# Kernel tuning notes

Measured on AMD Instinct MI355X. Metric: run time of the kernel, lower is better.

Reference implementation:

```python
import jax, jax.numpy as jnp
import numpy as np

N_STEPS = 5
N_ETYPES = 4
N_GRAPHS = 64
HEADS = 2
N, E, D = 50000, 600000, 128
C = 32


def setup_inputs() -> dict:
    key = jax.random.key(0)
    ks = jax.random.split(key, 24)
    s = 0.08  # param scale to keep activations well-conditioned
    return {
        "in_feat1": jax.random.normal(ks[0], (N, D), jnp.float32),
        "in_feat2": jax.random.normal(ks[1], (N, D), jnp.float32),
        "src1": jax.random.randint(ks[2], (E,), 0, N, jnp.int32),
        "dst1": jax.random.randint(ks[3], (E,), 0, N, jnp.int32),
        "etype1": jax.random.randint(ks[4], (E,), 0, N_ETYPES, jnp.int32),
        "gid1": jnp.sort(jax.random.randint(ks[5], (N,), 0, N_GRAPHS, jnp.int32)),
        "src2": jax.random.randint(ks[6], (E,), 0, N, jnp.int32),
        "dst2": jax.random.randint(ks[7], (E,), 0, N, jnp.int32),
        "etype2": jax.random.randint(ks[8], (E,), 0, N_ETYPES, jnp.int32),
        "gid2": jnp.sort(jax.random.randint(ks[9], (N,), 0, N_GRAPHS, jnp.int32)),
        "W_et": jax.random.normal(ks[10], (N_ETYPES, D, D), jnp.float32) * s,
        "b_et": jax.random.normal(ks[11], (N_ETYPES, D), jnp.float32) * s,
        "W_ih": jax.random.normal(ks[12], (3 * D, D), jnp.float32) * s,
        "W_hh": jax.random.normal(ks[13], (3 * D, D), jnp.float32) * s,
        "b_ih": jax.random.normal(ks[14], (3 * D,), jnp.float32) * s,
        "b_hh": jax.random.normal(ks[15], (3 * D,), jnp.float32) * s,
        "W_fc": jax.random.normal(ks[16], (HEADS * D, D), jnp.float32) * s,
        "attn_l": jax.random.normal(ks[17], (HEADS, D), jnp.float32) * s,
        "attn_r": jax.random.normal(ks[18], (HEADS, D), jnp.float32) * s,
        "gat_bias": jax.random.normal(ks[19], (HEADS * D,), jnp.float32) * s,
        "W_cls": jax.random.normal(ks[20], (C, D), jnp.float32) * s,
        "b_cls": jax.random.normal(ks[21], (C,), jnp.float32) * s,
    }


def _ggann(feat, src, dst, etype, gid,
           W_et, b_et, W_ih, W_hh, b_ih, b_hh,
           W_fc, attn_l, attn_r, gat_bias, W_cls, b_cls):
    n = feat.shape[0]
    h = feat  # in_feats == out_feats -> no zero-padding needed
    # ---- GatedGraphConv: n_steps of per-etype message passing + GRU ----
    for _ in range(N_STEPS):
        # per-etype linear on all nodes: [K, N, D]
        t = jnp.einsum('kod,nd->kno', W_et, h) + b_et[:, None, :]
        msg = t[etype, src]                         # [E, D] gather by (etype, src)
        a = jax.ops.segment_sum(msg, dst, num_segments=n)  # [N, D]
        # GRUCell(a, h)
        gi = a @ W_ih.T + b_ih                      # [N, 3D]
        gh = h @ W_hh.T + b_hh
        i_r, i_z, i_n = jnp.split(gi, 3, axis=1)
        h_r, h_z, h_n = jnp.split(gh, 3, axis=1)
        r = jax.nn.sigmoid(i_r + h_r)
        z = jax.nn.sigmoid(i_z + h_z)
        nn_ = jnp.tanh(i_n + r * h_n)
        h = (1.0 - z) * nn_ + z * h
    # F.normalize (L2 over dim=1) then sigmoid
    h = h / jnp.maximum(jnp.linalg.norm(h, axis=1, keepdims=True), 1e-12)
    h = jax.nn.sigmoid(h)
    # ---- GATConv (num_heads=2) ----
    zft = (h @ W_fc.T).reshape(n, HEADS, D)         # [N, H, D]
    el = jnp.sum(zft * attn_l[None], axis=-1)       # [N, H]
    er = jnp.sum(zft * attn_r[None], axis=-1)
    e = jax.nn.leaky_relu(el[src] + er[dst], 0.2)   # [E, H]
    m = jax.ops.segment_max(e, dst, num_segments=n)
    ex = jnp.exp(e - m[dst])
    den = jax.ops.segment_sum(ex, dst, num_segments=n)
    alpha = ex / den[dst]                           # edge softmax per dst, per head
    rst = jax.ops.segment_sum(alpha[:, :, None] * zft[src], dst, num_segments=n)
    rst = rst + gat_bias.reshape(1, HEADS, D)
    h = jax.nn.relu(rst)                            # [N, H, D] (dropout = eval identity)
    # ---- mean_nodes per graph + classify ----
    sums = jax.ops.segment_sum(h, gid, num_segments=N_GRAPHS)      # [B, H, D]
    cnt = jax.ops.segment_sum(jnp.ones((n, 1, 1), h.dtype), gid, num_segments=N_GRAPHS)
    hg = sums / jnp.maximum(cnt, 1.0)
    return hg @ W_cls.T + b_cls                     # [B, H, C]


def reference(in_feat1, in_feat2, src1, dst1, etype1, gid1,
              src2, dst2, etype2, gid2,
              W_et, b_et, W_ih, W_hh, b_ih, b_hh,
              W_fc, attn_l, attn_r, gat_bias, W_cls, b_cls):
    params = (W_et, b_et, W_ih, W_hh, b_ih, b_hh,
              W_fc, attn_l, attn_r, gat_bias, W_cls, b_cls)
    h1 = _ggann(in_feat1, src1, dst1, etype1, gid1, *params)  # [B, H, C]
    h2 = _ggann(in_feat2, src2, dst2, etype2, gid2, *params)
    # F.pairwise_distance(p=2, eps=1e-6) over last dim -> [B, H]
    dist = jnp.linalg.norm(h1 - h2 + 1e-6, axis=-1)
    return jax.nn.softmax(dist, axis=1)             # softmax over the 2 heads
```

## Files before the change

### kernel.cpp

```cpp
#include <hip/hip_runtime.h>
#include <math.h>

#define D 128
#define NG 64
#define NG2 128
#define NSTEPS 5

using short8 = __attribute__((ext_vector_type(8))) short;
using f32x4  = __attribute__((ext_vector_type(4))) float;
using f32x2  = __attribute__((ext_vector_type(2))) float;

__device__ __forceinline__ float sigf(float x) {
  float e = __expf(-fabsf(x));
  float inv = __fdividef(1.f, 1.f + e);
  return x >= 0.f ? inv : e * inv;
}
__device__ __forceinline__ float tanhf_fast(float x) {
  float e = __expf(-2.f * fabsf(x));
  float r = (1.f - e) * __fdividef(1.f, 1.f + e);
  return x >= 0.f ? r : -r;
}
__device__ __forceinline__ float lrelu(float x) { return x > 0.f ? x : 0.2f * x; }
__device__ __forceinline__ short f2bf(float x) {
  unsigned u = __float_as_uint(x);
  u += 0x7fff + ((u >> 16) & 1);
  return (short)(u >> 16);
}
__device__ __forceinline__ unsigned pk2(float x, float y) {
  return ((unsigned)(unsigned short)f2bf(y) << 16) | (unsigned short)f2bf(x);
}
__device__ __forceinline__ float bflo(unsigned v) { return __uint_as_float(v << 16); }
__device__ __forceinline__ float bfhi(unsigned v) { return __uint_as_float(v & 0xffff0000u); }
__device__ __forceinline__ float bf2f(short s) {
  return __uint_as_float(((unsigned)(unsigned short)s) << 16);
}
__device__ __forceinline__ unsigned char f2fp8(float x) {
  int p = __builtin_amdgcn_cvt_pk_fp8_f32(x, x, 0, false);
  return (unsigned char)(p & 0xff);
}

__device__ __forceinline__ void packK128(const float* __restrict__ W,
                                         short* __restrict__ P, int i) {
  int j = i & 7;
  int lane = (i >> 3) & 63;
  int kt = (i >> 9) & 3;
  int nt = i >> 11;
  int c = nt * 16 + (lane & 15);
  int k = kt * 32 + ((lane >> 4) << 3) + j;
  P[i] = f2bf(W[c * 128 + k]);
}
__device__ __forceinline__ void packA512f(const float* __restrict__ W_et,
                                          short* __restrict__ P, int i) {
  int j = i & 7;
  int lane = (i >> 3) & 63;
  int kt = (i >> 9) & 15;
  int nt = i >> 13;
  int c = nt * 16 + (lane & 15);
  int k = kt * 32 + ((lane >> 4) << 3) + j;
  P[i] = f2bf(W_et[(k >> 7) * 16384 + c * 128 + (k & 127)]);
}

__global__ __launch_bounds__(256) void k_setup(const float* __restrict__ W_et,
    const float* __restrict__ W_ih, const float* __restrict__ W_hh,
    const float* __restrict__ W_fc, const float* __restrict__ f1,
    const float* __restrict__ f2, short* __restrict__ WaP, short* __restrict__ WihP,
    short* __restrict__ WhhP, short* __restrict__ WfcP, short* __restrict__ hb,
    unsigned char* __restrict__ hq,
    int* __restrict__ deg, int* __restrict__ gcnt, int N2, int Nd4) {
  const int sA = 65536, sB = 49152, sC = 49152, sD = 32768;
  int sE = N2, sF = NG2;
  long sG = 2L * Nd4;
  long tot = (long)(sA + sB + sC + sD) + sE + sF + sG;
  for (long ii = (long)blockIdx.x * blockDim.x + threadIdx.x; ii < tot;
       ii += (long)gridDim.x * blockDim.x) {
    long r = ii;
    if (r < sA) { packA512f(W_et, WaP, (int)r); continue; }
    r -= sA;
    if (r < sB) { packK128(W_ih, WihP, (int)r); continue; }
    r -= sB;
    if (r < sC) { packK128(W_hh, WhhP, (int)r); continue; }
    r -= sC;
    if (r < sD) { packK128(W_fc, WfcP, (int)r); continue; }
    r -= sD;
    if (r < sE) { deg[r] = 0; continue; }
    r -= sE;
    if (r < sF) { gcnt[r] = 0; continue; }
    r -= sF;
    {
      int i = (int)r;
      float4 v = (i < Nd4) ? ((const float4*)f1)[i] : ((const float4*)f2)[i - Nd4];
      ((uint2*)hb)[i] = make_uint2(pk2(v.x, v.y), pk2(v.z, v.w));
      int q = __builtin_amdgcn_cvt_pk_fp8_f32(v.x, v.y, 0, false);
      q = __builtin_amdgcn_cvt_pk_fp8_f32(v.z, v.w, q, true);
      ((unsigned*)hq)[i] = (unsigned)q;
    }
  }
}

__global__ __launch_bounds__(256) void k_histgid(const int* __restrict__ dst1,
    const int* __restrict__ dst2, const int* __restrict__ gid1,
    const int* __restrict__ gid2, int E, int N, int* __restrict__ deg,
    int* __restrict__ gidc, int* __restrict__ gcnt, int EB, int N2) {
  __shared__ int cnt[NG2];
  if ((int)blockIdx.x < EB) {
    int slice = blockIdx.x & 7;
    int bls = blockIdx.x >> 3;
    int nbs = EB >> 3;
    int W = (N2 + 7) >> 3;
    int lo = slice * W, hi = lo + W;
    for (int e = bls * 256 + threadIdx.x; e < 2 * E; e += nbs * 256) {
      int d = (e < E) ? dst1[e] : dst2[e - E] + N;
      if (d >= lo && d < hi) atomicAdd(&deg[d], 1);
    }
  } else {
    int t = threadIdx.x;
    if (t < NG2) cnt[t] = 0;
    __syncthreads();
    int i = (blockIdx.x - EB) * 256 + t;
    if (i < 2 * N) {
      int g = (i < N) ? gid1[i] : gid2[i - N] + NG;
      gidc[i] = g;
      atomicAdd(&cnt[g], 1);
    }
    __syncthreads();
    if (t < NG2 && cnt[t]) atomicAdd(&gcnt[t], cnt[t]);
  }
}

__global__ __launch_bounds__(256) void k_scan_a(const int* __restrict__ deg, int n,
                                                int* __restrict__ bsum) {
  int base = blockIdx.x * 1024 + threadIdx.x * 4;
  int s = 0;
  if (base + 3 < n) {
    int4 v = *(const int4*)(deg + base);
    s = v.x + v.y + v.z + v.w;
  } else {
    for (int k = 0; k < 4; ++k) if (base + k < n) s += deg[base + k];
  }
  #pragma unroll
  for (int off = 32; off; off >>= 1) s += __shfl_xor(s, off);
  __shared__ int ws[4];
  if ((threadIdx.x & 63) == 0) ws[threadIdx.x >> 6] = s;
  __syncthreads();
  if (threadIdx.x == 0) bsum[blockIdx.x] = ws[0] + ws[1] + ws[2] + ws[3];
}

__global__ __launch_bounds__(1024) void k_scan_b(const int* __restrict__ bsum,
                                                 int* __restrict__ boffs, int nb) {
  int tid = threadIdx.x;
  int v = (tid < nb) ? bsum[tid] : 0;
  int lane = tid & 63, wv = tid >> 6;
  int x = v;
  #pragma unroll
  for (int off = 1; off < 64; off <<= 1) {
    int y = __shfl_up(x, off);
    if (lane >= off) x += y;
  }
  __shared__ int wsum[16];
  if (lane == 63) wsum[wv] = x;
  __syncthreads();
  if (tid < 16) {
    int u = wsum[tid];
    #pragma unroll
    for (int off = 1; off < 16; off <<= 1) {
      int y = __shfl_up(u, off);
      if (tid >= off) u += y;
    }
    wsum[tid] = u;
  }
  __syncthreads();
  int woff = wv ? wsum[wv - 1] : 0;
  if (tid < nb) boffs[tid] = woff + x - v;
}

__global__ __launch_bounds__(256) void k_scan_c(const int* __restrict__ deg,
    const int* __restrict__ boffs, int* __restrict__ row_ofs,
    int* __restrict__ cursor, int n) {
  int base = blockIdx.x * 1024 + threadIdx.x * 4;
  int v[4] = {0, 0, 0, 0};
  if (base + 3 < n) {
    int4 t = *(const int4*)(deg + base);
    v[0] = t.x; v[1] = t.y; v[2] = t.z; v[3] = t.w;
  } else {
    for (int k = 0; k < 4; ++k) if (base + k < n) v[k] = deg[base + k];
  }
  int s = v[0] + v[1] + v[2] + v[3];
  int lane = threadIdx.x & 63, wv = threadIdx.x >> 6;
  int x = s;
  #pragma unroll
  for (int off = 1; off < 64; off <<= 1) {
    int y = __shfl_up(x, off);
    if (lane >= off) x += y;
  }
  __shared__ int wsum[4];
  if (lane == 63) wsum[wv] = x;
  __syncthreads();
  int woff = 0;
  for (int w = 0; w < wv; ++w) woff += wsum[w];
  int run = boffs[blockIdx.x] + woff + x - s;
  #pragma unroll
  for (int k = 0; k < 4; ++k) {
    int i = base + k;
    if (i < n) {
      cursor[i] = run;
      run += v[k];
      row_ofs[i + 1] = run;
    }
  }
  if (blockIdx.x == 0 && threadIdx.x == 0) row_ofs[0] = 0;
}

__global__ __launch_bounds__(256) void k_scatter(const int* __restrict__ src1,
    const int* __restrict__ dst1, const int* __restrict__ ety1,
    const int* __restrict__ src2, const int* __restrict__ dst2,
    const int* __restrict__ ety2, int E, int N, int* __restrict__ cursor,
    int* __restrict__ csr_se, int N2) {
  int slice = blockIdx.x & 7;
  int bls = blockIdx.x >> 3;
  int nbs = gridDim.x >> 3;
  int W = (N2 + 7) >> 3;
  int lo = slice * W, hi = lo + W;
  for (int e = bls * 256 + threadIdx.x; e < 2 * E; e += nbs * 256) {
    int d = (e < E) ? dst1[e] : dst2[e - E] + N;
    if (d < lo || d >= hi) continue;
    int s, et;
    if (e < E) { s = src1[e]; et = ety1[e]; }
    else { s = src2[e - E] + N; et = ety2[e - E]; }
    int p = atomicAdd(&cursor[d], 1);
    csr_se[p] = (s << 10) + et;
  }
}

__global__ __launch_bounds__(1024) void k_aggemm(const unsigned char* __restrict__ hq,
    const int* __restrict__ row_ofs, const int* __restrict__ csr_se,
    const short* __restrict__ WaP, const float* __restrict__ b_et,
    short* __restrict__ ab, int M) {
  __shared__ short Stile[16 * 512];
  __shared__ float lcnt[16][4];
  int tid = threadIdx.x;
  int lane = tid & 63, wave = tid >> 6;
  int row0 = blockIdx.x * 16;

  int li = wave;
  int node = row0 + li;
  f32x2 A0 = {0.f, 0.f}, A1 = {0.f, 0.f}, A2 = {0.f, 0.f}, A3 = {0.f, 0.f};
  int c0 = 0, c1 = 0, c2 = 0, c3 = 0;
  const char* hqb = (const char*)hq;
  if (node < M) {
    int beg = row_ofs[node], end = row_ofs[node + 1];
    #define ACC(ET, V) do { \
        f32x2 t_ = __builtin_amdgcn_cvt_pk_f32_fp8((unsigned)(V), false); \
        if (ET == 0)      { A0 += t_; ++c0; } \
        else if (ET == 1) { A1 += t_; ++c1; } \
        else if (ET == 2) { A2 += t_; ++c2; } \
        else              { A3 += t_; ++c3; } } while (0)
    for (int base = beg; base < end; base += 64) {
      int nv = end - base; if (nv > 64) nv = 64;
      int r = (lane < nv) ? csr_se[base + lane] : 0;
      int j = 0;
      for (; j + 16 <= nv; j += 16) {
        int rr[16];
        #pragma unroll
        for (int k = 0; k < 16; ++k) rr[k] = __builtin_amdgcn_readlane(r, j + k);
        unsigned short v[16];
        #pragma unroll
        for (int k = 0; k < 16; ++k)
          v[k] = ((const unsigned short*)(hqb + (rr[k] >> 3)))[lane];
        #pragma unroll
        for (int k = 0; k < 16; ++k) ACC(rr[k] & 3, v[k]);
      }
      for (; j + 8 <= nv; j += 8) {
        int rr[8];
        #pragma unroll
        for (int k = 0; k < 8; ++k) rr[k] = __builtin_amdgcn_readlane(r, j + k);
        unsigned short v[8];
        #pragma unroll
        for (int k = 0; k < 8; ++k)
          v[k] = ((const unsigned short*)(hqb + (rr[k] >> 3)))[lane];
        #pragma unroll
        for (int k = 0; k < 8; ++k) ACC(rr[k] & 3, v[k]);
      }
      for (; j + 4 <= nv; j += 4) {
        int rr[4];
        #pragma unroll
        for (int k = 0; k < 4; ++k) rr[k] = __builtin_amdgcn_readlane(r, j + k);
        unsigned short v[4];
        #pragma unroll
        for (int k = 0; k < 4; ++k)
          v[k] = ((const unsigned short*)(hqb + (rr[k] >> 3)))[lane];
        #pragma unroll
        for (int k = 0; k < 4; ++k) ACC(rr[k] & 3, v[k]);
      }
      for (; j < nv; ++j) {
        int rr = __builtin_amdgcn_readlane(r, j);
        unsigned short v = ((const unsigned short*)(hqb + (rr >> 3)))[lane];
        ACC(rr & 3, v);
      }
    }
    #undef ACC
  }
  {
    int swz = (li & 7) << 4;
    unsigned* ld = (unsigned*)Stile;
    ld[(li * 1024 + ((lane * 4      ) ^ swz)) >> 2] = pk2(A0[0], A0[1]);
    ld[(li * 1024 + ((lane * 4 + 256) ^ swz)) >> 2] = pk2(A1[0], A1[1]);
    ld[(li * 1024 + ((lane * 4 + 512) ^ swz)) >> 2] = pk2(A2[0], A2[1]);
    ld[(li * 1024 + ((lane * 4 + 768) ^ swz)) >> 2] = pk2(A3[0], A3[1]);
    if (lane == 0) {
      lcnt[li][0] = (float)c0; lcnt[li][1] = (float)c1;
      lcnt[li][2] = (float)c2; lcnt[li][3] = (float)c3;
    }
  }
  __syncthreads();

  if (wave < 8) {
    int quad = lane >> 4, l15 = lane & 15;
    int swz = (l15 & 7) << 4;
    int nt = wave;
    f32x4 acc = {0.f, 0.f, 0.f, 0.f};
    #pragma unroll
    for (int kt = 0; kt < 16; ++kt) {
      int boff = l15 * 1024 + ((kt * 64 + quad * 16) ^ swz);
      short8 a = *(const short8*)((const char*)Stile + boff);
      short8 b = *(const short8*)(WaP + (((size_t)(nt * 16 + kt) * 64) + lane) * 8);
      acc = __builtin_amdgcn_mfma_f32_16x16x32_bf16(a, b, acc, 0, 0, 0);
    }
    int c = nt * 16 + l15;
    float be0 = b_et[c], be1 = b_et[128 + c], be2 = b_et[256 + c], be3 = b_et[384 + c];
    #pragma unroll
    for (int reg = 0; reg < 4; ++reg) {
      int lr = quad * 4 + reg;
      int r = row0 + lr;
      if (r < M) {
        float v = acc[reg] + lcnt[lr][0] * be0 + lcnt[lr][1] * be1
                           + lcnt[lr][2] * be2 + lcnt[lr][3] * be3;
        ab[(size_t)r * 128 + c] = f2bf(v);
      }
    }
  }
}

__global__ __launch_bounds__(256) void k_gru_mfma(const short* __restrict__ ab,
    short* __restrict__ hb, unsigned char* __restrict__ hq,
    const short* __restrict__ Pih, const short* __restrict__ Phh,
    const float* __restrict__ b_ih, const float* __restrict__ b_hh, int M) {
  __shared__ short hbs[4][16 * 128];
  __shared__ unsigned char hqs[4][16 * 128];
  int tid = threadIdx.x;
  int lane = tid & 63, wave = tid >> 6;
  int row0 = blockIdx.x * 64 + wave * 16;
  int quad = lane >> 4, l15 = lane & 15;
  short8 fa[4], fh[4];
  int ar = row0 + l15; if (ar >= M) ar = M - 1;
  #pragma unroll
  for (int kt = 0; kt < 4; ++kt) {
    fa[kt] = *(const short8*)(ab + (size_t)ar * 128 + kt * 32 + quad * 8);
    fh[kt] = *(const short8*)(hb + (size_t)ar * 128 + kt * 32 + quad * 8);
  }
  for (int nt = 0; nt < 8; ++nt) {
    f32x4 accr = {0.f,0.f,0.f,0.f}, accz = {0.f,0.f,0.f,0.f};
    f32x4 acci = {0.f,0.f,0.f,0.f}, acch = {0.f,0.f,0.f,0.f};
    #pragma unroll
    for (int kt = 0; kt < 4; ++kt) {
      size_t li = ((size_t)lane) * 8;
      short8 wr = *(const short8*)(Pih + ((size_t)((nt     ) * 4 + kt) * 64) * 8 + li);
      short8 wz = *(const short8*)(Pih + ((size_t)((nt +  8) * 4 + kt) * 64) * 8 + li);
      short8 wn = *(const short8*)(Pih + ((size_t)((nt + 16) * 4 + kt) * 64) * 8 + li);
      short8 ur = *(const short8*)(Phh + ((size_t)((nt     ) * 4 + kt) * 64) * 8 + li);
      short8 uz = *(const short8*)(Phh + ((size_t)((nt +  8) * 4 + kt) * 64) * 8 + li);
      short8 un = *(const short8*)(Phh + ((size_t)((nt + 16) * 4 + kt) * 64) * 8 + li);
      accr = __builtin_amdgcn_mfma_f32_16x16x32_bf16(fa[kt], wr, accr, 0, 0, 0);
      accr = __builtin_amdgcn_mfma_f32_16x16x32_bf16(fh[kt], ur, accr, 0, 0, 0);
      accz = __builtin_amdgcn_mfma_f32_16x16x32_bf16(fa[kt], wz, accz, 0, 0, 0);
      accz = __builtin_amdgcn_mfma_f32_16x16x32_bf16(fh[kt], uz, accz, 0, 0, 0);
      acci = __builtin_amdgcn_mfma_f32_16x16x32_bf16(fa[kt], wn, acci, 0, 0, 0);
      acch = __builtin_amdgcn_mfma_f32_16x16x32_bf16(fh[kt], un, acch, 0, 0, 0);
    }
    int c = nt * 16 + l15;
    float bir = b_ih[c],      bhr = b_hh[c];
    float biz = b_ih[c+128],  bhz = b_hh[c+128];
    float bin_= b_ih[c+256],  bhn = b_hh[c+256];
    #pragma unroll
    for (int reg = 0; reg < 4; ++reg) {
      int lr = quad * 4 + reg;
      int r = row0 + lr;
      float rg = sigf(accr[reg] + bir + bhr);
      float zg = sigf(accz[reg] + biz + bhz);
      float ng = tanhf_fast(acci[reg] + bin_ + rg * (acch[reg] + bhn));
      float hold = (r < M) ? bf2f(hb[(size_t)r * 128 + c]) : 0.f;
      float hn2 = (1.f - zg) * ng + zg * hold;
      hbs[wave][lr * 128 + c] = f2bf(hn2);
      hqs[wave][lr * 128 + c] = f2fp8(hn2);
    }
  }
  size_t gbase = (size_t)row0 * 128;
  #pragma unroll
  for (int i = 0; i < 4; ++i) {
    int gshort = i * 512 + lane * 8;
    int grow = gshort >> 7;
    if (row0 + grow < M) {
      uint4 v = *(const uint4*)&hbs[wave][gshort];
      *(uint4*)(hb + gbase + gshort) = v;
    }
  }
  #pragma unroll
  for (int i = 0; i < 2; ++i) {
    int gbyte = i * 1024 + lane * 16;
    int grow = gbyte >> 7;
    if (row0 + grow < M) {
      uint4 v = *(const uint4*)&hqs[wave][gbyte];
      *(uint4*)(hq + gbase + gbyte) = v;
    }
  }
}

__global__ __launch_bounds__(256) void k_fc_eler(const short* __restrict__ Ab,
    const short* __restrict__ Bp, const float* __restrict__ attn_l,
    const float* __restrict__ attn_r, unsigned char* __restrict__ zq,
    float* __restrict__ el, float* __restrict__ er, int M) {
  int tid = threadIdx.x;
  int lane = tid & 63, wave = tid >> 6;
  int row0 = blockIdx.x * 128 + wave * 32;
  int quad = lane >> 4, l15 = lane & 15;
  short8 af[2][4];
  #pragma unroll
  for (int rt = 0; rt < 2; ++rt) {
    int ar = row0 + rt * 16 + l15; if (ar >= M) ar = M - 1;
    #pragma unroll
    for (int kt = 0; kt < 4; ++kt)
      af[rt][kt] = *(const short8*)(Ab + (size_t)ar * 128 + kt * 32 + quad * 8);
  }
  #pragma unroll
  for (int rt = 0; rt < 2; ++rt) {
    float ss = 0.f;
    #pragma unroll
    for (int kt = 0; kt < 4; ++kt)
      #pragma unroll
      for (int j = 0; j < 8; ++j) {
        float x = bf2f(af[rt][kt][j]);
        ss += x * x;
      }
    ss += __shfl_xor(ss, 16);
    ss += __shfl_xor(ss, 32);
    float inv = 1.f / fmaxf(sqrtf(ss), 1e-12f);
    #pragma unroll
    for (int kt = 0; kt < 4; ++kt)
      #pragma unroll
      for (int j = 0; j < 8; ++j)
        af[rt][kt][j] = f2bf(sigf(bf2f(af[rt][kt][j]) * inv));
  }
  float elp[2][2][4] = {};
  float erp[2][2][4] = {};
  for (int nt = 0; nt < 16; ++nt) {
    f32x4 a0 = {0.f,0.f,0.f,0.f}, a1 = {0.f,0.f,0.f,0.f};
    #pragma unroll
    for (int kt = 0; kt < 4; ++kt) {
      short8 b = *(const short8*)(Bp + (((size_t)(nt * 4 + kt) * 64) + lane) * 8);
      a0 = __builtin_amdgcn_mfma_f32_16x16x32_bf16(af[0][kt], b, a0, 0, 0, 0);
      a1 = __builtin_amdgcn_mfma_f32_16x16x32_bf16(af[1][kt], b, a1, 0, 0, 0);
    }
    int head = nt >> 3;
    int colh = (nt & 7) * 16 + l15;
    float alv = attn_l[head * 128 + colh];
    float arv = attn_r[head * 128 + colh];
    int c = nt * 16 + l15;
    #pragma unroll
    for (int rt = 0; rt < 2; ++rt) {
      f32x4 acc = rt ? a1 : a0;
      #pragma unroll
      for (int reg = 0; reg < 4; ++reg) {
        int r = row0 + rt * 16 + quad * 4 + reg;
        if (r < M) zq[(size_t)r * 256 + c] = f2fp8(acc[reg]);
        elp[rt][head][reg] += acc[reg] * alv;
        erp[rt][head][reg] += acc[reg] * arv;
      }
    }
  }
  #pragma unroll
  for (int off = 1; off < 16; off <<= 1) {
    #pragma unroll
    for (int rt = 0; rt < 2; ++rt)
      #pragma unroll
      for (int h = 0; h < 2; ++h)
        #pragma unroll
        for (int reg = 0; reg < 4; ++reg) {
          elp[rt][h][reg] += __shfl_xor(elp[rt][h][reg], off);
          erp[rt][h][reg] += __shfl_xor(erp[rt][h][reg], off);
        }
  }
  if (l15 == 0) {
    #pragma unroll
    for (int rt = 0; rt < 2; ++rt)
      #pragma unroll
      for (int h = 0; h < 2; ++h)
        #pragma unroll
        for (int reg = 0; reg < 4; ++reg) {
          int r = row0 + rt * 16 + quad * 4 + reg;
          if (r < M) {
            el[r * 2 + h] = elp[rt][h][reg];
            er[r * 2 + h] = erp[rt][h][reg];
          }
        }
  }
}

__global__ __launch_bounds__(256) void k_gat(const unsigned char* __restrict__ zq,
    const float* __restrict__ el, const float* __restrict__ er,
    const int* __restrict__ row_ofs, const int* __restrict__ csr_se,
    const float* __restrict__ gat_bias, short* __restrict__ outb,
    float* __restrict__ sums, int N) {
  if (blockIdx.x < NG2) sums[blockIdx.x * 256 + threadIdx.x] = 0.f;
  int node = blockIdx.x * 4 + (threadIdx.x >> 6);
  int lane = threadIdx.x & 63;
  if (node >= N) return;
  int beg = row_ofs[node], end = row_ofs[node + 1];
  float2 ern = ((const float2*)er)[node];
  float l0 = 0.f, l1 = 0.f;
  float4 acc = {0.f, 0.f, 0.f, 0.f};
  int head = lane >> 5;
  const char* elb = (const char*)el;
  const char* zqb = (const char*)zq;
  for (int base = beg; base < end; base += 64) {
    int nv = end - base; if (nv > 64) nv = 64;
    int se = (lane < nv) ? csr_se[base + lane] : 0;
    float p0 = 0.f, p1 = 0.f;
    if (lane < nv) {
      float2 els = *(const float2*)(elb + (se >> 7));
      p0 = expf(lrelu(els.x + ern.x));
      p1 = expf(lrelu(els.y + ern.y));
    }
    float t0 = p0, t1 = p1;
    #pragma unroll
    for (int off = 32; off; off >>= 1) { t0 += __shfl_xor(t0, off); t1 += __shfl_xor(t1, off); }
    l0 += t0; l1 += t1;
    int w01 = (int)pk2(p0, p1);
    int j = 0;
    for (; j + 8 <= nv; j += 8) {
      int bb[8]; unsigned ww[8];
      #pragma unroll
      for (int k = 0; k < 8; ++k) {
        bb[k] = __builtin_amdgcn_readlane(se, j + k) >> 2;
        ww[k] = (unsigned)__builtin_amdgcn_readlane(w01, j + k);
      }
      unsigned zz[8];
      #pragma unroll
      for (int k = 0; k < 8; ++k)
        zz[k] = ((const unsigned*)(zqb + bb[k]))[lane];
      #pragma unroll
      for (int k = 0; k < 8; ++k) {
        float f = head ? bfhi(ww[k]) : bflo(ww[k]);
        f32x2 lo = __builtin_amdgcn_cvt_pk_f32_fp8(zz[k], false);
        f32x2 hi = __builtin_amdgcn_cvt_pk_f32_fp8(zz[k], true);
        acc.x += f * lo[0]; acc.y += f * lo[1];
        acc.z += f * hi[0]; acc.w += f * hi[1];
      }
    }
    for (; j + 4 <= nv; j += 4) {
      int bb[4]; unsigned ww[4];
      #pragma unroll
      for (int k = 0; k < 4; ++k) {
        bb[k] = __builtin_amdgcn_readlane(se, j + k) >> 2;
        ww[k] = (unsigned)__builtin_amdgcn_readlane(w01, j + k);
      }
      unsigned zz[4];
      #pragma unroll
      for (int k = 0; k < 4; ++k)
        zz[k] = ((const unsigned*)(zqb + bb[k]))[lane];
      #pragma unroll
      for (int k = 0; k < 4; ++k) {
        float f = head ? bfhi(ww[k]) : bflo(ww[k]);
        f32x2 lo = __builtin_amdgcn_cvt_pk_f32_fp8(zz[k], false);
        f32x2 hi = __builtin_amdgcn_cvt_pk_f32_fp8(zz[k], true);
        acc.x += f * lo[0]; acc.y += f * lo[1];
        acc.z += f * hi[0]; acc.w += f * hi[1];
      }
    }
    for (; j < nv; ++j) {
      int bj = __builtin_amdgcn_readlane(se, j) >> 2;
      unsigned wj = (unsigned)__builtin_amdgcn_readlane(w01, j);
      float w = head ? bfhi(wj) : bflo(wj);
      unsigned zv = ((const unsigned*)(zqb + bj))[lane];
      f32x2 lo = __builtin_amdgcn_cvt_pk_f32_fp8(zv, false);
      f32x2 hi = __builtin_amdgcn_cvt_pk_f32_fp8(zv, true);
      acc.x += w * lo[0]; acc.y += w * lo[1];
      acc.z += w * hi[0]; acc.w += w * hi[1];
    }
  }
  float inv0 = (l0 > 0.f) ? 1.f / l0 : 0.f;
  float inv1 = (l1 > 0.f) ? 1.f / l1 : 0.f;
  float inv = head ? inv1 : inv0;
  float4 b = ((const float4*)gat_bias)[lane];
  float ox = fmaxf(acc.x * inv + b.x, 0.f);
  float oy = fmaxf(acc.y * inv + b.y, 0.f);
  float oz = fmaxf(acc.z * inv + b.z, 0.f);
  float ow = fmaxf(acc.w * inv + b.w, 0.f);
  ((uint2*)(outb + (size_t)node * 256))[lane] = make_uint2(pk2(ox, oy), pk2(oz, ow));
}

__global__ __launch_bounds__(256) void k_segred(const short* __restrict__ hgatb,
    const int* __restrict__ gidc, float* __restrict__ sums, int NT2) {
  int node0 = blockIdx.x * 128;
  int col = threadIdx.x;
  int end = node0 + 128; if (end > NT2) end = NT2;
  if (node0 >= NT2) return;
  float acc = 0.f;
  int gcur = gidc[node0];
  for (int n = node0; n < end; ++n) {
    int g = gidc[n];
    if (g != gcur) {
      atomicAdd(&sums[gcur * 256 + col], acc);
      acc = 0.f; gcur = g;
    }
    acc += bf2f(hgatb[(size_t)n * 256 + col]);
  }
  atomicAdd(&sums[gcur * 256 + col], acc);
}

__global__ __launch_bounds__(64) void k_classify(const float* __restrict__ sums,
    const int* __restrict__ gcnt, const float* __restrict__ W_cls,
    const float* __restrict__ b_cls, float* __restrict__ logits) {
  int g = blockIdx.x, tid = threadIdx.x;
  int hh = tid >> 5, c = tid & 31;
  float invc = 1.f / fmaxf((float)gcnt[g], 1.f);
  float acc = 0.f;
  for (int d = 0; d < D; ++d)
    acc += (sums[g * 256 + hh * D + d] * invc) * W_cls[c * D + d];
  logits[g * 64 + hh * 32 + c] = acc + b_cls[c];
}

__global__ __launch_bounds__(64) void k_final(const float* __restrict__ logits,
    float* __restrict__ out) {
  int g = threadIdx.x;
  if (g >= NG) return;
  float d[2];
  #pragma unroll
  for (int hh = 0; hh < 2; ++hh) {
    float s = 0.f;
    for (int c = 0; c < 32; ++c) {
      float df = logits[g * 64 + hh * 32 + c] - logits[(g + NG) * 64 + hh * 32 + c] + 1e-6f;
      s += df * df;
    }
    d[hh] = sqrtf(s);
  }
  float mx = fmaxf(d[0], d[1]);
  float e0 = expf(d[0] - mx), e1 = expf(d[1] - mx);
  float den = e0 + e1;
  out[g * 2] = e0 / den;
  out[g * 2 + 1] = e1 / den;
}

extern "C" void kernel_launch(void* const* d_in, const int* in_sizes, int n_in,
                              void* d_out, int out_size, void* d_ws, size_t ws_size,
                              hipStream_t stream) {
  const float* in_feat1 = (const float*)d_in[0];
  const float* in_feat2 = (const float*)d_in[1];
  const int* src1 = (const int*)d_in[2];
  const int* dst1 = (const int*)d_in[3];
  const int* ety1 = (const int*)d_in[4];
  const int* gid1 = (const int*)d_in[5];
  const int* src2 = (const int*)d_in[6];
  const int* dst2 = (const int*)d_in[7];
  const int* ety2 = (const int*)d_in[8];
  const int* gid2 = (const int*)d_in[9];
  const float* W_et = (const float*)d_in[10];
  const float* b_et = (const float*)d_in[11];
  const float* W_ih = (const float*)d_in[12];
  const float* W_hh = (const float*)d_in[13];
  const float* b_ih = (const float*)d_in[14];
  const float* b_hh = (const float*)d_in[15];
  const float* W_fc = (const float*)d_in[16];
  const float* attn_l = (const float*)d_in[17];
  const float* attn_r = (const float*)d_in[18];
  const float* gat_bias = (const float*)d_in[19];
  const float* W_cls = (const float*)d_in[20];
  const float* b_cls = (const float*)d_in[21];
  float* out = (float*)d_out;

  int N = in_sizes[0] / D;
  int E = in_sizes[2];
  int N2 = 2 * N, E2 = 2 * E;

  char* p = (char*)d_ws;
  auto alloc = [&](size_t bytes) -> void* {
    char* r = p;
    p += (bytes + 255) & ~(size_t)255;
    return (void*)r;
  };
  short* WaP  = (short*)alloc((size_t)512 * 128 * 2);
  short* WihP = (short*)alloc((size_t)384 * 128 * 2);
  short* WhhP = (short*)alloc((size_t)384 * 128 * 2);
  short* WfcP = (short*)alloc((size_t)256 * 128 * 2);
  short* hb  = (short*)alloc((size_t)N2 * D * 2);
  unsigned char* hq = (unsigned char*)alloc((size_t)N2 * D);
  short* ab  = (short*)alloc((size_t)N2 * D * 2);
  short* hgatb = (short*)alloc((size_t)N2 * 256 * 2);
  unsigned char* zq = (unsigned char*)alloc((size_t)N2 * 256);
  float* el  = (float*)alloc((size_t)N2 * 2 * 4);
  float* er  = (float*)alloc((size_t)N2 * 2 * 4);
  float* sums= (float*)alloc((size_t)NG2 * 256 * 4);
  float* logits = (float*)alloc((size_t)NG2 * 64 * 4);
  int* deg     = (int*)alloc((size_t)N2 * 4);
  int* row_ofs = (int*)alloc(((size_t)N2 + 1) * 4);
  int* cursor  = (int*)alloc((size_t)N2 * 4);
  int* gidc    = (int*)alloc((size_t)N2 * 4);
  int* gcnt    = (int*)alloc((size_t)NG2 * 4);
  int* bsum    = (int*)alloc((size_t)1024 * 4);
  int* boffs   = (int*)alloc((size_t)1024 * 4);
  int* csr_se  = (int*)alloc((size_t)E2 * 4);
  if ((size_t)(p - (char*)d_ws) > ws_size) return;

  k_setup<<<dim3(2048), dim3(256), 0, stream>>>(W_et, W_ih, W_hh, W_fc,
      in_feat1, in_feat2, WaP, WihP, WhhP, WfcP, hb, hq, deg, gcnt, N2, N * D / 4);

  int EB = 4800;
  int GB = (N2 + 255) / 256;
  int nb = (N2 + 1023) / 1024;
  k_histgid<<<dim3(EB + GB), dim3(256), 0, stream>>>(dst1, dst2, gid1, gid2,
                                                     E, N, deg, gidc, gcnt, EB, N2);
  k_scan_a<<<dim3(nb), dim3(256), 0, stream>>>(deg, N2, bsum);
  k_scan_b<<<dim3(1), dim3(1024), 0, stream>>>(bsum, boffs, nb);
  k_scan_c<<<dim3(nb), dim3(256), 0, stream>>>(deg, boffs, row_ofs, cursor, N2);
  k_scatter<<<dim3(4800), dim3(256), 0, stream>>>(src1, dst1, ety1, src2, dst2, ety2,
                                                  E, N, cursor, csr_se, N2);

  int gb16 = (N2 + 15) / 16;
  int gb64 = (N2 + 63) / 64;
  int gb128 = (N2 + 127) / 128;
  int nb4 = (N2 + 3) / 4;

  for (int s = 0; s < NSTEPS; ++s) {
    k_aggemm<<<dim3(gb16), dim3(1024), 0, stream>>>(hq, row_ofs, csr_se, WaP, b_et, ab, N2);
    k_gru_mfma<<<dim3(gb64), dim3(256), 0, stream>>>(ab, hb, hq, WihP, WhhP, b_ih, b_hh, N2);
  }
  k_fc_eler<<<dim3(gb128), dim3(256), 0, stream>>>(hb, WfcP, attn_l, attn_r, zq, el, er, N2);
  k_gat<<<dim3(nb4), dim3(256), 0, stream>>>(zq, el, er, row_ofs, csr_se,
                                             gat_bias, hgatb, sums, N2);
  k_segred<<<dim3((N2 + 127) / 128), dim3(256), 0, stream>>>(hgatb, gidc, sums, N2);
  k_classify<<<dim3(NG2), dim3(64), 0, stream>>>(sums, gcnt, W_cls, b_cls, logits);
  k_final<<<dim3(1), dim3(64), 0, stream>>>(logits, out);
}
```

Baseline: 1.184 ms.

## Partition GRU kernel waves by output columns to keep weights in registers

The GRU MFMA kernel now assigns each wave two 16-column output tiles across all 64 rows of the block, instead of 16 rows across all 128 columns. Each wave loads its slice of the six gate weight matrices into registers once and reuses it for four row groups. Before, every wave re-read the whole weight set from global memory. The cost is that the activation rows are now read by all four waves (four times per block), the new state is staged in a shared 64-row buffer that needs a block-wide barrier before the store, and register pressure rises from holding 24 weight fragments.

```diff
diff --git a/kernel.cpp b/kernel.cpp
--- a/kernel.cpp
+++ b/kernel.cpp
@@ -344,72 +344,79 @@
     short* __restrict__ hb, unsigned char* __restrict__ hq,
     const short* __restrict__ Pih, const short* __restrict__ Phh,
     const float* __restrict__ b_ih, const float* __restrict__ b_hh, int M) {
-  __shared__ short hbs[4][16 * 128];
-  __shared__ unsigned char hqs[4][16 * 128];
+  __shared__ short hbs[64 * 128];
+  __shared__ unsigned char hqs[64 * 128];
   int tid = threadIdx.x;
   int lane = tid & 63, wave = tid >> 6;
-  int row0 = blockIdx.x * 64 + wave * 16;
+  int row0 = blockIdx.x * 64;
   int quad = lane >> 4, l15 = lane & 15;
-  short8 fa[4], fh[4];
-  int ar = row0 + l15; if (ar >= M) ar = M - 1;
-  #pragma unroll
-  for (int kt = 0; kt < 4; ++kt) {
-    fa[kt] = *(const short8*)(ab + (size_t)ar * 128 + kt * 32 + quad * 8);
-    fh[kt] = *(const short8*)(hb + (size_t)ar * 128 + kt * 32 + quad * 8);
-  }
-  for (int nt = 0; nt < 8; ++nt) {
-    f32x4 accr = {0.f,0.f,0.f,0.f}, accz = {0.f,0.f,0.f,0.f};
-    f32x4 acci = {0.f,0.f,0.f,0.f}, acch = {0.f,0.f,0.f,0.f};
+  size_t li = ((size_t)lane) * 8;
+
+  #pragma unroll
+  for (int t = 0; t < 2; ++t) {
+    int nt = wave * 2 + t;
+    short8 wr[4], wz[4], wn[4], ur[4], uz[4], un[4];
     #pragma unroll
     for (int kt = 0; kt < 4; ++kt) {
-      size_t li = ((size_t)lane) * 8;
-      short8 wr = *(const short8*)(Pih + ((size_t)((nt     ) * 4 + kt) * 64) * 8 + li);
-      short8 wz = *(const short8*)(Pih + ((size_t)((nt +  8) * 4 + kt) * 64) * 8 + li);
-      short8 wn = *(const short8*)(Pih + ((size_t)((nt + 16) * 4 + kt) * 64) * 8 + li);
-      short8 ur = *(const short8*)(Phh + ((size_t)((nt     ) * 4 + kt) * 64) * 8 + li);
-      short8 uz = *(const short8*)(Phh + ((size_t)((nt +  8) * 4 + kt) * 64) * 8 + li);
-      short8 un = *(const short8*)(Phh + ((size_t)((nt + 16) * 4 + kt) * 64) * 8 + li);
-      accr = __builtin_amdgcn_mfma_f32_16x16x32_bf16(fa[kt], wr, accr, 0, 0, 0);
-      accr = __builtin_amdgcn_mfma_f32_16x16x32_bf16(fh[kt], ur, accr, 0, 0, 0);
-      accz = __builtin_amdgcn_mfma_f32_16x16x32_bf16(fa[kt], wz, accz, 0, 0, 0);
-      accz = __builtin_amdgcn_mfma_f32_16x16x32_bf16(fh[kt], uz, accz, 0, 0, 0);
-      acci = __builtin_amdgcn_mfma_f32_16x16x32_bf16(fa[kt], wn, acci, 0, 0, 0);
-      acch = __builtin_amdgcn_mfma_f32_16x16x32_bf16(fh[kt], un, acch, 0, 0, 0);
+      wr[kt] = *(const short8*)(Pih + ((size_t)((nt     ) * 4 + kt) * 64) * 8 + li);
+      wz[kt] = *(const short8*)(Pih + ((size_t)((nt +  8) * 4 + kt) * 64) * 8 + li);
+      wn[kt] = *(const short8*)(Pih + ((size_t)((nt + 16) * 4 + kt) * 64) * 8 + li);
+      ur[kt] = *(const short8*)(Phh + ((size_t)((nt     ) * 4 + kt) * 64) * 8 + li);
+      uz[kt] = *(const short8*)(Phh + ((size_t)((nt +  8) * 4 + kt) * 64) * 8 + li);
+      un[kt] = *(const short8*)(Phh + ((size_t)((nt + 16) * 4 + kt) * 64) * 8 + li);
     }
     int c = nt * 16 + l15;
     float bir = b_ih[c],      bhr = b_hh[c];
     float biz = b_ih[c+128],  bhz = b_hh[c+128];
     float bin_= b_ih[c+256],  bhn = b_hh[c+256];
     #pragma unroll
-    for (int reg = 0; reg < 4; ++reg) {
-      int lr = quad * 4 + reg;
-      int r = row0 + lr;
-      float rg = sigf(accr[reg] + bir + bhr);
-      float zg = sigf(accz[reg] + biz + bhz);
-      float ng = tanhf_fast(acci[reg] + bin_ + rg * (acch[reg] + bhn));
-      float hold = (r < M) ? bf2f(hb[(size_t)r * 128 + c]) : 0.f;
-      float hn2 = (1.f - zg) * ng + zg * hold;
-      hbs[wave][lr * 128 + c] = f2bf(hn2);
-      hqs[wave][lr * 128 + c] = f2fp8(hn2);
-    }
-  }
+    for (int rg = 0; rg < 4; ++rg) {
+      int ar = row0 + rg * 16 + l15; if (ar >= M) ar = M - 1;
+      f32x4 accr = {0.f,0.f,0.f,0.f}, accz = {0.f,0.f,0.f,0.f};
+      f32x4 acci = {0.f,0.f,0.f,0.f}, acch = {0.f,0.f,0.f,0.f};
+      #pragma unroll
+      for (int kt = 0; kt < 4; ++kt) {
+        short8 fa = *(const short8*)(ab + (size_t)ar * 128 + kt * 32 + quad * 8);
+        short8 fh = *(const short8*)(hb + (size_t)ar * 128 + kt * 32 + quad * 8);
+        accr = __builtin_amdgcn_mfma_f32_16x16x32_bf16(fa, wr[kt], accr, 0, 0, 0);
+        accr = __builtin_amdgcn_mfma_f32_16x16x32_bf16(fh, ur[kt], accr, 0, 0, 0);
+        accz = __builtin_amdgcn_mfma_f32_16x16x32_bf16(fa, wz[kt], accz, 0, 0, 0);
+        accz = __builtin_amdgcn_mfma_f32_16x16x32_bf16(fh, uz[kt], accz, 0, 0, 0);
+        acci = __builtin_amdgcn_mfma_f32_16x16x32_bf16(fa, wn[kt], acci, 0, 0, 0);
+        acch = __builtin_amdgcn_mfma_f32_16x16x32_bf16(fh, un[kt], acch, 0, 0, 0);
+      }
+      #pragma unroll
+      for (int reg = 0; reg < 4; ++reg) {
+        int lr = rg * 16 + quad * 4 + reg;
+        int r = row0 + lr;
+        float rgate = sigf(accr[reg] + bir + bhr);
+        float zg = sigf(accz[reg] + biz + bhz);
+        float ng = tanhf_fast(acci[reg] + bin_ + rgate * (acch[reg] + bhn));
+        float hold = (r < M) ? bf2f(hb[(size_t)r * 128 + c]) : 0.f;
+        float hn2 = (1.f - zg) * ng + zg * hold;
+        hbs[lr * 128 + c] = f2bf(hn2);
+        hqs[lr * 128 + c] = f2fp8(hn2);
+      }
+    }
+  }
+  __syncthreads();
   size_t gbase = (size_t)row0 * 128;
   #pragma unroll
   for (int i = 0; i < 4; ++i) {
-    int gshort = i * 512 + lane * 8;
-    int grow = gshort >> 7;
+    int off16 = i * 2048 + tid * 8;
+    int grow = off16 >> 7;
     if (row0 + grow < M) {
-      uint4 v = *(const uint4*)&hbs[wave][gshort];
-      *(uint4*)(hb + gbase + gshort) = v;
+      uint4 v = *(const uint4*)&hbs[off16];
+      *(uint4*)(hb + gbase + off16) = v;
     }
   }
   #pragma unroll
   for (int i = 0; i < 2; ++i) {
-    int gbyte = i * 1024 + lane * 16;
-    int grow = gbyte >> 7;
+    int offb = i * 4096 + tid * 16;
+    int grow = offb >> 7;
     if (row0 + grow < M) {
-      uint4 v = *(const uint4*)&hqs[wave][gbyte];
-      *(uint4*)(hq + gbase + gbyte) = v;
+      uint4 v = *(const uint4*)&hqs[offb];
+      *(uint4*)(hq + gbase + offb) = v;
     }
   }
 }
```

After: 1.215 ms. 1.03x slower.

## Fuse aggregation GEMM and GRU into one per-step kernel with ping-pong buffers

Applied to the files above, without the earlier changes.

Merges the per-etype aggregation + W_et GEMM kernel and the GRU MFMA kernel into a single k_step kernel. The aggregated tile and the old hidden state stay in LDS, so the bf16 `ab` intermediate never makes a round trip through global memory, and one launch per step is removed. Double-buffered hb/hq arrays avoid the read/write race on neighbour features within a step. The trade-offs are more LDS per block, GRU work done by only 8 of 16 waves, and blocks of 16 rows instead of 64, which reloads the GRU weights more often.

```diff
diff --git a/kernel.cpp b/kernel.cpp
--- a/kernel.cpp
+++ b/kernel.cpp
@@ -231,75 +231,83 @@
   }
 }
 
-__global__ __launch_bounds__(1024) void k_aggemm(const unsigned char* __restrict__ hq,
+__global__ __launch_bounds__(1024) void k_step(const unsigned char* __restrict__ hq_old,
+    const short* __restrict__ hb_old, unsigned char* __restrict__ hq_new,
+    short* __restrict__ hb_new,
     const int* __restrict__ row_ofs, const int* __restrict__ csr_se,
     const short* __restrict__ WaP, const float* __restrict__ b_et,
-    short* __restrict__ ab, int M) {
+    const short* __restrict__ Pih, const short* __restrict__ Phh,
+    const float* __restrict__ b_ih, const float* __restrict__ b_hh, int M) {
   __shared__ short Stile[16 * 512];
   __shared__ float lcnt[16][4];
+  __shared__ short abt[16 * 128];
+  __shared__ short hin[16 * 128];
+  __shared__ short hbs[16 * 128];
+  __shared__ unsigned char hqs[16 * 128];
   int tid = threadIdx.x;
   int lane = tid & 63, wave = tid >> 6;
   int row0 = blockIdx.x * 16;
-
-  int li = wave;
-  int node = row0 + li;
-  f32x2 A0 = {0.f, 0.f}, A1 = {0.f, 0.f}, A2 = {0.f, 0.f}, A3 = {0.f, 0.f};
-  int c0 = 0, c1 = 0, c2 = 0, c3 = 0;
-  const char* hqb = (const char*)hq;
-  if (node < M) {
-    int beg = row_ofs[node], end = row_ofs[node + 1];
-    #define ACC(ET, V) do { \
-        f32x2 t_ = __builtin_amdgcn_cvt_pk_f32_fp8((unsigned)(V), false); \
-        if (ET == 0)      { A0 += t_; ++c0; } \
-        else if (ET == 1) { A1 += t_; ++c1; } \
-        else if (ET == 2) { A2 += t_; ++c2; } \
-        else              { A3 += t_; ++c3; } } while (0)
-    for (int base = beg; base < end; base += 64) {
-      int nv = end - base; if (nv > 64) nv = 64;
-      int r = (lane < nv) ? csr_se[base + lane] : 0;
-      int j = 0;
-      for (; j + 16 <= nv; j += 16) {
-        int rr[16];
-        #pragma unroll
-        for (int k = 0; k < 16; ++k) rr[k] = __builtin_amdgcn_readlane(r, j + k);
-        unsigned short v[16];
-        #pragma unroll
-        for (int k = 0; k < 16; ++k)
-          v[k] = ((const unsigned short*)(hqb + (rr[k] >> 3)))[lane];
-        #pragma unroll
-        for (int k = 0; k < 16; ++k) ACC(rr[k] & 3, v[k]);
+  int quad = lane >> 4, l15 = lane & 15;
+
+  {
+    int li = wave;
+    int node = row0 + li;
+    f32x2 A0 = {0.f, 0.f}, A1 = {0.f, 0.f}, A2 = {0.f, 0.f}, A3 = {0.f, 0.f};
+    int c0 = 0, c1 = 0, c2 = 0, c3 = 0;
+    const char* hqb = (const char*)hq_old;
+    if (node < M) {
+      int beg = row_ofs[node], end = row_ofs[node + 1];
+      #define ACC(ET, V) do { \
+          f32x2 t_ = __builtin_amdgcn_cvt_pk_f32_fp8((unsigned)(V), false); \
+          if (ET == 0)      { A0 += t_; ++c0; } \
+          else if (ET == 1) { A1 += t_; ++c1; } \
+          else if (ET == 2) { A2 += t_; ++c2; } \
+          else              { A3 += t_; ++c3; } } while (0)
+      for (int base = beg; base < end; base += 64) {
+        int nv = end - base; if (nv > 64) nv = 64;
+        int r = (lane < nv) ? csr_se[base + lane] : 0;
+        int j = 0;
+        for (; j + 16 <= nv; j += 16) {
+          int rr[16];
+          #pragma unroll
+          for (int k = 0; k < 16; ++k) rr[k] = __builtin_amdgcn_readlane(r, j + k);
+          unsigned short v[16];
+          #pragma unroll
+          for (int k = 0; k < 16; ++k)
+            v[k] = ((const unsigned short*)(hqb + (rr[k] >> 3)))[lane];
+          #pragma unroll
+          for (int k = 0; k < 16; ++k) ACC(rr[k] & 3, v[k]);
+        }
+        for (; j + 8 <= nv; j += 8) {
+          int rr[8];
+          #pragma unroll
+          for (int k = 0; k < 8; ++k) rr[k] = __builtin_amdgcn_readlane(r, j + k);
+          unsigned short v[8];
+          #pragma unroll
+          for (int k = 0; k < 8; ++k)
+            v[k] = ((const unsigned short*)(hqb + (rr[k] >> 3)))[lane];
+          #pragma unroll
+          for (int k = 0; k < 8; ++k) ACC(rr[k] & 3, v[k]);
+        }
+        for (; j + 4 <= nv; j += 4) {
+          int rr[4];
+          #pragma unroll
+          for (int k = 0; k < 4; ++k) rr[k] = __builtin_amdgcn_readlane(r, j + k);
+          unsigned short v[4];
+          #pragma unroll
+          for (int k = 0; k < 4; ++k)
+            v[k] = ((const unsigned short*)(hqb + (rr[k] >> 3)))[lane];
+          #pragma unroll
+          for (int k = 0; k < 4; ++k) ACC(rr[k] & 3, v[k]);
+        }
+        for (; j < nv; ++j) {
+          int rr = __builtin_amdgcn_readlane(r, j);
+          unsigned short v = ((const unsigned short*)(hqb + (rr >> 3)))[lane];
+          ACC(rr & 3, v);
+        }
       }
-      for (; j + 8 <= nv; j += 8) {
-        int rr[8];
-        #pragma unroll
-        for (int k = 0; k < 8; ++k) rr[k] = __builtin_amdgcn_readlane(r, j + k);
-        unsigned short v[8];
-        #pragma unroll
-        for (int k = 0; k < 8; ++k)
-          v[k] = ((const unsigned short*)(hqb + (rr[k] >> 3)))[lane];
-        #pragma unroll
-        for (int k = 0; k < 8; ++k) ACC(rr[k] & 3, v[k]);
-      }
-      for (; j + 4 <= nv; j += 4) {
-        int rr[4];
-        #pragma unroll
-        for (int k = 0; k < 4; ++k) rr[k] = __builtin_amdgcn_readlane(r, j + k);
-        unsigned short v[4];
-        #pragma unroll
-        for (int k = 0; k < 4; ++k)
-          v[k] = ((const unsigned short*)(hqb + (rr[k] >> 3)))[lane];
-        #pragma unroll
-        for (int k = 0; k < 4; ++k) ACC(rr[k] & 3, v[k]);
-      }
-      for (; j < nv; ++j) {
-        int rr = __builtin_amdgcn_readlane(r, j);
-        unsigned short v = ((const unsigned short*)(hqb + (rr >> 3)))[lane];
-        ACC(rr & 3, v);
-      }
-    }
-    #undef ACC
-  }
-  {
+      #undef ACC
+    }
     int swz = (li & 7) << 4;
     unsigned* ld = (unsigned*)Stile;
     ld[(li * 1024 + ((lane * 4      ) ^ swz)) >> 2] = pk2(A0[0], A0[1]);
@@ -314,7 +322,6 @@
   __syncthreads();
 
   if (wave < 8) {
-    int quad = lane >> 4, l15 = lane & 15;
     int swz = (l15 & 7) << 4;
     int nt = wave;
     f32x4 acc = {0.f, 0.f, 0.f, 0.f};
@@ -330,51 +337,45 @@
     #pragma unroll
     for (int reg = 0; reg < 4; ++reg) {
       int lr = quad * 4 + reg;
-      int r = row0 + lr;
-      if (r < M) {
-        float v = acc[reg] + lcnt[lr][0] * be0 + lcnt[lr][1] * be1
-                           + lcnt[lr][2] * be2 + lcnt[lr][3] * be3;
-        ab[(size_t)r * 128 + c] = f2bf(v);
-      }
-    }
-  }
-}
-
-__global__ __launch_bounds__(256) void k_gru_mfma(const short* __restrict__ ab,
-    short* __restrict__ hb, unsigned char* __restrict__ hq,
-    const short* __restrict__ Pih, const short* __restrict__ Phh,
-    const float* __restrict__ b_ih, const float* __restrict__ b_hh, int M) {
-  __shared__ short hbs[4][16 * 128];
-  __shared__ unsigned char hqs[4][16 * 128];
-  int tid = threadIdx.x;
-  int lane = tid & 63, wave = tid >> 6;
-  int row0 = blockIdx.x * 64 + wave * 16;
-  int quad = lane >> 4, l15 = lane & 15;
-  short8 fa[4], fh[4];
-  int ar = row0 + l15; if (ar >= M) ar = M - 1;
-  #pragma unroll
-  for (int kt = 0; kt < 4; ++kt) {
-    fa[kt] = *(const short8*)(ab + (size_t)ar * 128 + kt * 32 + quad * 8);
-    fh[kt] = *(const short8*)(hb + (size_t)ar * 128 + kt * 32 + quad * 8);
-  }
-  for (int nt = 0; nt < 8; ++nt) {
+      float v = acc[reg] + lcnt[lr][0] * be0 + lcnt[lr][1] * be1
+                         + lcnt[lr][2] * be2 + lcnt[lr][3] * be3;
+      int bo = (lr * 256 + c * 2) ^ ((lr & 7) << 4);
+      *(short*)((char*)abt + bo) = f2bf(v);
+    }
+  } else if (wave < 12) {
+    int t2 = tid - 512;
+    int row = t2 >> 4;
+    int col8 = t2 & 15;
+    int r = row0 + row;
+    uint4 v = make_uint4(0, 0, 0, 0);
+    if (r < M) v = *(const uint4*)(hb_old + (size_t)r * 128 + col8 * 8);
+    int bo = (row * 256 + col8 * 16) ^ ((row & 7) << 4);
+    *(uint4*)((char*)hin + bo) = v;
+  }
+  __syncthreads();
+
+  if (wave < 8) {
+    int nt = wave;
+    size_t li = ((size_t)lane) * 8;
     f32x4 accr = {0.f,0.f,0.f,0.f}, accz = {0.f,0.f,0.f,0.f};
     f32x4 acci = {0.f,0.f,0.f,0.f}, acch = {0.f,0.f,0.f,0.f};
     #pragma unroll
     for (int kt = 0; kt < 4; ++kt) {
-      size_t li = ((size_t)lane) * 8;
+      int ao = (l15 * 256 + (kt * 64 + quad * 16)) ^ ((l15 & 7) << 4);
+      short8 fa = *(const short8*)((const char*)abt + ao);
+      short8 fh = *(const short8*)((const char*)hin + ao);
       short8 wr = *(const short8*)(Pih + ((size_t)((nt     ) * 4 + kt) * 64) * 8 + li);
       short8 wz = *(const short8*)(Pih + ((size_t)((nt +  8) * 4 + kt) * 64) * 8 + li);
       short8 wn = *(const short8*)(Pih + ((size_t)((nt + 16) * 4 + kt) * 64) * 8 + li);
       short8 ur = *(const short8*)(Phh + ((size_t)((nt     ) * 4 + kt) * 64) * 8 + li);
       short8 uz = *(const short8*)(Phh + ((size_t)((nt +  8) * 4 + kt) * 64) * 8 + li);
       short8 un = *(const short8*)(Phh + ((size_t)((nt + 16) * 4 + kt) * 64) * 8 + li);
-      accr = __builtin_amdgcn_mfma_f32_16x16x32_bf16(fa[kt], wr, accr, 0, 0, 0);
-      accr = __builtin_amdgcn_mfma_f32_16x16x32_bf16(fh[kt], ur, accr, 0, 0, 0);
-      accz = __builtin_amdgcn_mfma_f32_16x16x32_bf16(fa[kt], wz, accz, 0, 0, 0);
-      accz = __builtin_amdgcn_mfma_f32_16x16x32_bf16(fh[kt], uz, accz, 0, 0, 0);
-      acci = __builtin_amdgcn_mfma_f32_16x16x32_bf16(fa[kt], wn, acci, 0, 0, 0);
-      acch = __builtin_amdgcn_mfma_f32_16x16x32_bf16(fh[kt], un, acch, 0, 0, 0);
+      accr = __builtin_amdgcn_mfma_f32_16x16x32_bf16(fa, wr, accr, 0, 0, 0);
+      accr = __builtin_amdgcn_mfma_f32_16x16x32_bf16(fh, ur, accr, 0, 0, 0);
+      accz = __builtin_amdgcn_mfma_f32_16x16x32_bf16(fa, wz, accz, 0, 0, 0);
+      accz = __builtin_amdgcn_mfma_f32_16x16x32_bf16(fh, uz, accz, 0, 0, 0);
+      acci = __builtin_amdgcn_mfma_f32_16x16x32_bf16(fa, wn, acci, 0, 0, 0);
+      acch = __builtin_amdgcn_mfma_f32_16x16x32_bf16(fh, un, acch, 0, 0, 0);
     }
     int c = nt * 16 + l15;
     float bir = b_ih[c],      bhr = b_hh[c];
@@ -383,34 +384,28 @@
     #pragma unroll
     for (int reg = 0; reg < 4; ++reg) {
       int lr = quad * 4 + reg;
-      int r = row0 + lr;
-      float rg = sigf(accr[reg] + bir + bhr);
+      float rgate = sigf(accr[reg] + bir + bhr);
       float zg = sigf(accz[reg] + biz + bhz);
-      float ng = tanhf_fast(acci[reg] + bin_ + rg * (acch[reg] + bhn));
-      float hold = (r < M) ? bf2f(hb[(size_t)r * 128 + c]) : 0.f;
+      float ng = tanhf_fast(acci[reg] + bin_ + rgate * (acch[reg] + bhn));
+      int ho = (lr * 256 + c * 2) ^ ((lr & 7) << 4);
+      float hold = bf2f(*(const short*)((const char*)hin + ho));
       float hn2 = (1.f - zg) * ng + zg * hold;
-      hbs[wave][lr * 128 + c] = f2bf(hn2);
-      hqs[wave][lr * 128 + c] = f2fp8(hn2);
-    }
-  }
-  size_t gbase = (size_t)row0 * 128;
-  #pragma unroll
-  for (int i = 0; i < 4; ++i) {
-    int gshort = i * 512 + lane * 8;
-    int grow = gshort >> 7;
-    if (row0 + grow < M) {
-      uint4 v = *(const uint4*)&hbs[wave][gshort];
-      *(uint4*)(hb + gbase + gshort) = v;
-    }
-  }
-  #pragma unroll
-  for (int i = 0; i < 2; ++i) {
-    int gbyte = i * 1024 + lane * 16;
-    int grow = gbyte >> 7;
-    if (row0 + grow < M) {
-      uint4 v = *(const uint4*)&hqs[wave][gbyte];
-      *(uint4*)(hq + gbase + gbyte) = v;
-    }
+      hbs[lr * 128 + c] = f2bf(hn2);
+      hqs[lr * 128 + c] = f2fp8(hn2);
+    }
+  }
+  __syncthreads();
+
+  if (tid < 256) {
+    int off16 = tid * 8;
+    int grow = off16 >> 7;
+    if (row0 + grow < M)
+      *(uint4*)(hb_new + (size_t)row0 * 128 + off16) = *(const uint4*)&hbs[off16];
+  } else if (tid < 384) {
+    int offb = (tid - 256) * 16;
+    int grow = offb >> 7;
+    if (row0 + grow < M)
+      *(uint4*)(hq_new + (size_t)row0 * 128 + offb) = *(const uint4*)&hqs[offb];
   }
 }
 
@@ -690,9 +685,10 @@
   short* WihP = (short*)alloc((size_t)384 * 128 * 2);
   short* WhhP = (short*)alloc((size_t)384 * 128 * 2);
   short* WfcP = (short*)alloc((size_t)256 * 128 * 2);
-  short* hb  = (short*)alloc((size_t)N2 * D * 2);
-  unsigned char* hq = (unsigned char*)alloc((size_t)N2 * D);
-  short* ab  = (short*)alloc((size_t)N2 * D * 2);
+  short* hb0 = (short*)alloc((size_t)N2 * D * 2);
+  short* hb1 = (short*)alloc((size_t)N2 * D * 2);
+  unsigned char* hq0 = (unsigned char*)alloc((size_t)N2 * D);
+  unsigned char* hq1 = (unsigned char*)alloc((size_t)N2 * D);
   short* hgatb = (short*)alloc((size_t)N2 * 256 * 2);
   unsigned char* zq = (unsigned char*)alloc((size_t)N2 * 256);
   float* el  = (float*)alloc((size_t)N2 * 2 * 4);
@@ -710,7 +706,7 @@
   if ((size_t)(p - (char*)d_ws) > ws_size) return;
 
   k_setup<<<dim3(2048), dim3(256), 0, stream>>>(W_et, W_ih, W_hh, W_fc,
-      in_feat1, in_feat2, WaP, WihP, WhhP, WfcP, hb, hq, deg, gcnt, N2, N * D / 4);
+      in_feat1, in_feat2, WaP, WihP, WhhP, WfcP, hb0, hq0, deg, gcnt, N2, N * D / 4);
 
   int EB = 4800;
   int GB = (N2 + 255) / 256;
@@ -724,15 +720,18 @@
                                                   E, N, cursor, csr_se, N2);
 
   int gb16 = (N2 + 15) / 16;
-  int gb64 = (N2 + 63) / 64;
   int gb128 = (N2 + 127) / 128;
   int nb4 = (N2 + 3) / 4;
 
+  short* hbp[2] = {hb0, hb1};
+  unsigned char* hqp[2] = {hq0, hq1};
   for (int s = 0; s < NSTEPS; ++s) {
-    k_aggemm<<<dim3(gb16), dim3(1024), 0, stream>>>(hq, row_ofs, csr_se, WaP, b_et, ab, N2);
-    k_gru_mfma<<<dim3(gb64), dim3(256), 0, stream>>>(ab, hb, hq, WihP, WhhP, b_ih, b_hh, N2);
-  }
-  k_fc_eler<<<dim3(gb128), dim3(256), 0, stream>>>(hb, WfcP, attn_l, attn_r, zq, el, er, N2);
+    k_step<<<dim3(gb16), dim3(1024), 0, stream>>>(
+        hqp[s & 1], hbp[s & 1], hqp[(s + 1) & 1], hbp[(s + 1) & 1],
+        row_ofs, csr_se, WaP, b_et, WihP, WhhP, b_ih, b_hh, N2);
+  }
+  short* hbf = hbp[NSTEPS & 1];
+  k_fc_eler<<<dim3(gb128), dim3(256), 0, stream>>>(hbf, WfcP, attn_l, attn_r, zq, el, er, N2);
   k_gat<<<dim3(nb4), dim3(256), 0, stream>>>(zq, el, er, row_ofs, csr_se,
                                              gat_bias, hgatb, sums, N2);
   k_segred<<<dim3((N2 + 127) / 128), dim3(256), 0, stream>>>(hgatb, gidc, sums, N2);
```

New measurement: 1.004 ms. 15.2% less time.
